# Optimization experiments

Hardware: AMD Instinct MI355X
Metric: run time of the kernel (lower is better)

The kernel has to match this reference:

```python
import jax, jax.numpy as jnp
import numpy as np

N = 100000; E = 1600000; G = 2000; S = 40; MAXP = 50
IN = 64; F = 128; H = 4; HD = F // H; FFN = 8 * F
EPS = 1e-5; BN_EPS = 1e-5

def _ln(x, g, b):
    m = jnp.mean(x, -1, keepdims=True)
    v = jnp.mean((x - m) ** 2, -1, keepdims=True)
    return (x - m) * jax.lax.rsqrt(v + EPS) * g + b

def setup_inputs():
    key = jax.random.key(0)
    ks = jax.random.split(key, 16)
    def lin(k, i, o):
        kw, kb = jax.random.split(k)
        lim = 1.0 / np.sqrt(i)
        return (jax.random.uniform(kw, (i, o), jnp.float32, -lim, lim),
                jax.random.uniform(kb, (o,), jnp.float32, -lim, lim))
    W_gcn, b_gcn = lin(ks[1], IN, F)
    Wq, bq = lin(ks[2], F, F); Wk, bk = lin(ks[3], F, F)
    Wv, bv = lin(ks[4], F, F); Wo, bo = lin(ks[5], F, F)
    W1, b1 = lin(ks[6], F, FFN); W2, b2 = lin(ks[7], FFN, F)
    Wg, bg = lin(ks[8], 2 * F, F)
    ones = lambda: jnp.ones((F,), jnp.float32)
    zeros = lambda: jnp.zeros((F,), jnp.float32)
    return {
        'x': jax.random.normal(ks[0], (N, IN), jnp.float32),
        'edge_index': jax.random.randint(ks[9], (2, E), 0, N),
        'batch': jnp.repeat(jnp.arange(G), N // G),
        'set_batch': jnp.repeat(jnp.arange(S), G // S),
        'W_gcn': W_gcn, 'b_gcn': b_gcn,
        'bn_g': ones(), 'bn_b': zeros(),
        'lnpre_g': ones(), 'lnpre_b': zeros(),
        'Wq': Wq, 'bq': bq, 'Wk': Wk, 'bk': bk, 'Wv': Wv, 'bv': bv, 'Wo': Wo, 'bo': bo,
        'ln1_g': ones(), 'ln1_b': zeros(),
        'W1': W1, 'b1': b1, 'W2': W2, 'b2': b2,
        'ln2_g': ones(), 'ln2_b': zeros(),
        'Wg': Wg, 'bg': bg,
    }

def _forward(x, W_gcn, b_gcn, bn_g, bn_b, lnpre_g, lnpre_b, Wq, bq, Wk, bk, Wv, bv, Wo, bo, ln1_g, ln1_b, W1, b1, W2, b2, ln2_g, ln2_b, Wg, bg, edge_index, batch, set_batch):
    row, col = edge_index[0], edge_index[1]
    # GCNConv, improved=True -> self-loop weight 2.0 (PyG gcn_norm)
    xw = x @ W_gcn                                              # [N,F]
    deg = jax.ops.segment_sum(jnp.ones(E, xw.dtype), col, N) + 2.0
    dinv = jax.lax.rsqrt(deg)
    norm = dinv[row] * dinv[col]                                # [E]
    agg = jax.ops.segment_sum(xw[row] * norm[:, None], col, N)  # scatter-add to targets
    h = agg + (2.0 * dinv * dinv)[:, None] * xw + b_gcn
    # BatchNorm1d eval (running_mean=0, running_var=1) + ReLU; dropout is identity in eval
    h = jax.nn.relu(h * jax.lax.rsqrt(jnp.asarray(1.0 + BN_EPS, h.dtype)) * bn_g + bn_b)
    # global mean pool per graph
    cnt_g = jax.ops.segment_sum(jnp.ones(N, h.dtype), batch, G)
    z = jax.ops.segment_sum(h, batch, G) / cnt_g[:, None]       # [G,F]
    # to_dense_batch over sets (set_batch is sorted)
    cnt_s = jax.ops.segment_sum(jnp.ones(G, jnp.int32), set_batch, S)
    starts = jnp.cumsum(cnt_s) - cnt_s
    pos = jnp.arange(G) - starts[set_batch]                     # position within set
    zd = jnp.zeros((S, MAXP, F), z.dtype).at[set_batch, pos].set(z)
    mask = jnp.arange(MAXP)[None, :] < cnt_s[:, None]           # [S,MAXP]
    # pre-LN MHA with key_padding_mask
    zn = _ln(zd, lnpre_g, lnpre_b)
    q = (zn @ Wq + bq).reshape(S, MAXP, H, HD)
    k = (zn @ Wk + bk).reshape(S, MAXP, H, HD)
    v = (zn @ Wv + bv).reshape(S, MAXP, H, HD)
    scores = jnp.einsum('sqhd,skhd->shqk', q, k) / np.sqrt(HD)
    scores = jnp.where(mask[:, None, None, :], scores, -1e9)
    attn = jax.nn.softmax(scores, -1)
    o = jnp.einsum('shqk,skhd->sqhd', attn, v).reshape(S, MAXP, F) @ Wo + bo
    zd = _ln(zd + o, ln1_g, ln1_b)
    # FFN block (post-LN residual)
    f = jax.nn.relu(zd @ W1 + b1) @ W2 + b2
    zd = _ln(zd + f, ln2_g, ln2_b)
    # z_dense[mask] ordering == gather via (set_batch, pos); broadcast to nodes
    set_info = zd[set_batch, pos][batch]                        # [N,F]
    # gated fusion
    gate = jax.nn.sigmoid(jnp.concatenate([h, set_info], -1) @ Wg + bg)
    return gate * set_info + (1.0 - gate) * h

def reference(x, edge_index, batch, set_batch, W_gcn, b_gcn, bn_g, bn_b, lnpre_g, lnpre_b, Wq, bq, Wk, bk, Wv, bv, Wo, bo, ln1_g, ln1_b, W1, b1, W2, b2, ln2_g, ln2_b, Wg, bg):
    return _forward(x, W_gcn, b_gcn, bn_g, bn_b, lnpre_g, lnpre_b, Wq, bq, Wk, bk, Wv, bv, Wo, bo, ln1_g, ln1_b, W1, b1, W2, b2, ln2_g, ln2_b, Wg, bg, edge_index, batch, set_batch)
```

## Files before the change

### kernel.cpp

```cpp
#include <hip/hip_runtime.h>
#include <hip/hip_bf16.h>
#include <cstddef>

#define NN 100000
#define NE 1600000
#define NG 2000
#define NS 40
#define INF 64
#define F 128
#define FFN_DIM 1024
#define NB 782
#define BCAP 3072
#define SC_BLOCKS 512
#define SC_CHUNK 3125
#define KSPLIT 8

using bf16 = __hip_bfloat16;
typedef __attribute__((ext_vector_type(8))) short short8;
typedef __attribute__((ext_vector_type(4))) float f32x4;
typedef __attribute__((ext_vector_type(2))) float f32x2;

__device__ __forceinline__ short f2bs(float f){
    union { bf16 b; short s; } u; u.b = __float2bfloat16(f); return u.s;
}
__device__ __forceinline__ unsigned int pk2(float a, float b){
    return (unsigned int)(unsigned short)f2bs(a) | ((unsigned int)(unsigned short)f2bs(b) << 16);
}

__global__ __launch_bounds__(1024) void k_binit(int* __restrict__ bcursor){
    int t = threadIdx.x;
    if (t < NB) bcursor[t] = t * BCAP;
}

__global__ __launch_bounds__(256) void k_xws(const float* __restrict__ x, const float* __restrict__ W,
                                             const float* __restrict__ dinv, unsigned char* __restrict__ xws8){
    __shared__ short Xs[128*72];
    __shared__ short Ws[128*72];
    int t = threadIdx.x;
    int rowBase = blockIdx.x * 128;
    #pragma unroll
    for (int i=0;i<32;i++){
        int id = i*256+t; int k = id>>7, n = id&127;
        Ws[n*72 + k] = f2bs(W[id]);
    }
    #pragma unroll
    for (int i=0;i<8;i++){
        int id = i*256+t;
        int r = id>>4; int k4 = (id&15)*4;
        int row = rowBase + r; if (row >= NN) row = NN-1;
        float4 v = *(const float4*)&x[(size_t)row*INF + k4];
        *(unsigned int*)&Xs[r*72 + k4]     = pk2(v.x, v.y);
        *(unsigned int*)&Xs[r*72 + k4 + 2] = pk2(v.z, v.w);
    }
    __syncthreads();
    int lane = t & 63, w = t >> 6;
    int lr = lane & 15, quad = lane >> 4;
    f32x4 acc[2][8];
    #pragma unroll
    for (int i=0;i<2;i++)
        #pragma unroll
        for (int j=0;j<8;j++) acc[i][j] = (f32x4){0.f,0.f,0.f,0.f};
    #pragma unroll
    for (int ks=0; ks<2; ++ks){
        int kb = ks*32 + quad*8;
        short8 b0 = *(const short8*)&Xs[((w  )*16 + lr)*72 + kb];
        short8 b1 = *(const short8*)&Xs[((w+4)*16 + lr)*72 + kb];
        #pragma unroll
        for (int mt=0; mt<8; ++mt){
            short8 a = *(const short8*)&Ws[(mt*16 + lr)*72 + kb];
            acc[0][mt] = __builtin_amdgcn_mfma_f32_16x16x32_bf16(a, b0, acc[0][mt], 0, 0, 0);
            acc[1][mt] = __builtin_amdgcn_mfma_f32_16x16x32_bf16(a, b1, acc[1][mt], 0, 0, 0);
        }
    }
    #pragma unroll
    for (int rt=0; rt<2; ++rt){
        int row = rowBase + (w + rt*4)*16 + lr;
        if (row < NN){
            float dv = dinv[row];
            #pragma unroll
            for (int mt=0; mt<8; ++mt){
                int p = __builtin_amdgcn_cvt_pk_fp8_f32(acc[rt][mt][0]*dv, acc[rt][mt][1]*dv, 0, false);
                p     = __builtin_amdgcn_cvt_pk_fp8_f32(acc[rt][mt][2]*dv, acc[rt][mt][3]*dv, p, true);
                *(int*)&xws8[(size_t)row*F + mt*16 + quad*4] = p;
            }
        }
    }
}

__global__ __launch_bounds__(1024) void k_scatter2(const int* __restrict__ ei, int* __restrict__ bcursor,
                                                   int* __restrict__ ebuf){
    __shared__ int lh[NB];
    __shared__ int lb[NB];
    int t = threadIdx.x;
    int base = blockIdx.x * SC_CHUNK;
    for (int b=t; b<NB; b+=1024) lh[b] = 0;
    __syncthreads();
    int rr[4], cc[4];
    #pragma unroll
    for (int q=0;q<4;q++){
        int i = t + q*1024;
        bool v = (i < SC_CHUNK);
        int idx = v ? (base + i) : base;
        rr[q] = ei[idx];
        cc[q] = ei[NE + idx];
        if (v) atomicAdd(&lh[cc[q]>>7], 1);
    }
    __syncthreads();
    for (int b=t; b<NB; b+=1024){
        int n = lh[b];
        lb[b] = n ? atomicAdd(&bcursor[b], n) : 0;
        lh[b] = 0;
    }
    __syncthreads();
    #pragma unroll
    for (int q=0;q<4;q++){
        int i = t + q*1024;
        if (i < SC_CHUNK){
            int b = cc[q] >> 7;
            int rk = atomicAdd(&lh[b], 1);
            ebuf[lb[b] + rk] = (rr[q] << 7) | (cc[q] & 127);
        }
    }
}

__global__ __launch_bounds__(256) void k_sort(const int* __restrict__ ebuf, const int* __restrict__ bcursor,
                                              int* __restrict__ cnt, float* __restrict__ dinv,
                                              int* __restrict__ nstart, int* __restrict__ ebuf2){
    __shared__ int lh[128];
    __shared__ int s[128];
    __shared__ int lcur[128];
    int t = threadIdx.x;
    int b = blockIdx.x;
    int e0 = b * BCAP;
    int nE = bcursor[b] - e0;
    if (t < 128) lh[t] = 0;
    __syncthreads();
    for (int i=t; i<nE; i+=256) atomicAdd(&lh[ebuf[e0+i] & 127], 1);
    __syncthreads();
    int c = (t < 128) ? lh[t] : 0;
    if (t < 128) s[t] = c;
    __syncthreads();
    #pragma unroll
    for (int off=1; off<128; off<<=1){
        int v = (t >= off && t < 128) ? s[t-off] : 0;
        __syncthreads();
        if (t < 128) s[t] += v;
        __syncthreads();
    }
    int node = b*128 + t;
    if (t < 128){
        int excl = s[t] - c;
        lcur[t] = excl;
        if (node < NN){
            nstart[node] = e0 + excl;
            cnt[node] = c;
            dinv[node] = rsqrtf((float)c + 2.0f);
        }
    }
    __syncthreads();
    for (int i=t; i<nE; i+=256){
        int v = ebuf[e0 + i];
        int nl = v & 127;
        int rk = atomicAdd(&lcur[nl], 1);
        ebuf2[e0 + rk] = (v >> 7) << 5;
    }
}

__global__ __launch_bounds__(256) void k_aggpool(const unsigned char* __restrict__ xws8,
                                                 const int* __restrict__ nstart, const int* __restrict__ cnt,
                                                 const float* __restrict__ dinv, const float* __restrict__ b_gcn,
                                                 const float* __restrict__ bn_g, const float* __restrict__ bn_b,
                                                 const int* __restrict__ ebuf2,
                                                 const float* __restrict__ lnpre_g, const float* __restrict__ lnpre_b,
                                                 float* __restrict__ h, unsigned short* __restrict__ hb,
                                                 float* __restrict__ z, float* __restrict__ zn,
                                                 unsigned short* __restrict__ znb){
    __shared__ float zacc[4][128];
    int t = threadIdx.x;
    int lane = t & 63, w = t >> 6;
    int half = lane >> 5, lh = lane & 31;
    int g = blockIdx.x;
    const unsigned int* xw32 = (const unsigned int*)xws8;
    unsigned int* hb32 = (unsigned int*)hb;
    unsigned int* znb32 = (unsigned int*)znb;

    float4 bg4  = *(const float4*)&b_gcn[4*lh];
    float4 bng4 = *(const float4*)&bn_g[4*lh];
    float4 bnb4 = *(const float4*)&bn_b[4*lh];
    const float bns = rsqrtf(1.f + 1e-5f);

    float za0=0.f, za1=0.f, za2=0.f, za3=0.f;

    for (int i = w; i < 50; i += 4){
        int node = g*50 + i;
        int s0n = nstart[node]; int dg = cnt[node]; float dv = dinv[node];
        unsigned int us = xw32[node*32 + lh];
        float a0=0.f, a1=0.f, a2=0.f, a3=0.f;
        int j=0;
        for (; j+8<=dg; j+=8){
            int r0 = ebuf2[s0n+j+0+half];
            int r1 = ebuf2[s0n+j+2+half];
            int r2 = ebuf2[s0n+j+4+half];
            int r3 = ebuf2[s0n+j+6+half];
            unsigned int u0 = xw32[r0 + lh];
            unsigned int u1 = xw32[r1 + lh];
            unsigned int u2 = xw32[r2 + lh];
            unsigned int u3 = xw32[r3 + lh];
            f32x2 l0 = __builtin_amdgcn_cvt_pk_f32_fp8(u0, false);
            f32x2 h0 = __builtin_amdgcn_cvt_pk_f32_fp8(u0, true);
            f32x2 l1 = __builtin_amdgcn_cvt_pk_f32_fp8(u1, false);
            f32x2 h1 = __builtin_amdgcn_cvt_pk_f32_fp8(u1, true);
            f32x2 l2 = __builtin_amdgcn_cvt_pk_f32_fp8(u2, false);
            f32x2 h2 = __builtin_amdgcn_cvt_pk_f32_fp8(u2, true);
            f32x2 l3 = __builtin_amdgcn_cvt_pk_f32_fp8(u3, false);
            f32x2 h3 = __builtin_amdgcn_cvt_pk_f32_fp8(u3, true);
            a0 += (l0.x + l1.x) + (l2.x + l3.x);
            a1 += (l0.y + l1.y) + (l2.y + l3.y);
            a2 += (h0.x + h1.x) + (h2.x + h3.x);
            a3 += (h0.y + h1.y) + (h2.y + h3.y);
        }
        for (; j+2<=dg; j+=2){
            int r0 = ebuf2[s0n+j+half];
            unsigned int u0 = xw32[r0 + lh];
            f32x2 l0 = __builtin_amdgcn_cvt_pk_f32_fp8(u0, false);
            f32x2 h0 = __builtin_amdgcn_cvt_pk_f32_fp8(u0, true);
            a0 += l0.x; a1 += l0.y; a2 += h0.x; a3 += h0.y;
        }
        if (j < dg && half == 0){
            int r0 = ebuf2[s0n+j];
            unsigned int u0 = xw32[r0 + lh];
            f32x2 l0 = __builtin_amdgcn_cvt_pk_f32_fp8(u0, false);
            f32x2 h0 = __builtin_amdgcn_cvt_pk_f32_fp8(u0, true);
            a0 += l0.x; a1 += l0.y; a2 += h0.x; a3 += h0.y;
        }
        a0 += __shfl_xor(a0, 32);
        a1 += __shfl_xor(a1, 32);
        a2 += __shfl_xor(a2, 32);
        a3 += __shfl_xor(a3, 32);
        f32x2 fl = __builtin_amdgcn_cvt_pk_f32_fp8(us, false);
        f32x2 fh = __builtin_amdgcn_cvt_pk_f32_fp8(us, true);
        float p0 = dv*(a0 + 2.f*fl.x) + bg4.x;
        float p1 = dv*(a1 + 2.f*fl.y) + bg4.y;
        float p2 = dv*(a2 + 2.f*fh.x) + bg4.z;
        float p3 = dv*(a3 + 2.f*fh.y) + bg4.w;
        p0 = fmaxf(p0*bns*bng4.x + bnb4.x, 0.f);
        p1 = fmaxf(p1*bns*bng4.y + bnb4.y, 0.f);
        p2 = fmaxf(p2*bns*bng4.z + bnb4.z, 0.f);
        p3 = fmaxf(p3*bns*bng4.w + bnb4.w, 0.f);
        if (half == 0){
            *(float4*)&h[(size_t)node*F + 4*lh] = make_float4(p0,p1,p2,p3);
            *(uint2*)&hb32[(size_t)node*64 + 2*lh] = make_uint2(pk2(p0,p1), pk2(p2,p3));
        }
        za0 += p0; za1 += p1; za2 += p2; za3 += p3;
    }
    if (half == 0)
        *(float4*)&zacc[w][4*lh] = make_float4(za0, za1, za2, za3);
    __syncthreads();
    if (w == 0){
        float4 v0 = *(const float4*)&zacc[0][4*lh];
        float4 v1 = *(const float4*)&zacc[1][4*lh];
        float4 v2 = *(const float4*)&zacc[2][4*lh];
        float4 v3 = *(const float4*)&zacc[3][4*lh];
        float s0 = ((v0.x+v1.x)+(v2.x+v3.x)) / 50.0f;
        float s1 = ((v0.y+v1.y)+(v2.y+v3.y)) / 50.0f;
        float s2 = ((v0.z+v1.z)+(v2.z+v3.z)) / 50.0f;
        float s3 = ((v0.w+v1.w)+(v2.w+v3.w)) / 50.0f;
        if (half == 0)
            *(float4*)&z[(size_t)g*F + 4*lh] = make_float4(s0,s1,s2,s3);
        float s = (s0+s1)+(s2+s3);
        #pragma unroll
        for (int off=1; off<32; off<<=1) s += __shfl_xor(s, off);
        float m = s * (1.f/128.f);
        float d0=s0-m, d1=s1-m, d2=s2-m, d3=s3-m;
        float vv = (d0*d0+d1*d1)+(d2*d2+d3*d3);
        #pragma unroll
        for (int off=1; off<32; off<<=1) vv += __shfl_xor(vv, off);
        float rs = rsqrtf(vv*(1.f/128.f) + 1e-5f);
        float4 lg = *(const float4*)&lnpre_g[4*lh];
        float4 lb = *(const float4*)&lnpre_b[4*lh];
        if (half == 0){
            float o0 = d0*rs*lg.x+lb.x, o1 = d1*rs*lg.y+lb.y;
            float o2 = d2*rs*lg.z+lb.z, o3 = d3*rs*lg.w+lb.w;
            *(float4*)&zn[(size_t)g*F + 4*lh] = make_float4(o0,o1,o2,o3);
            *(uint2*)&znb32[(size_t)g*64 + 2*lh] = make_uint2(pk2(o0,o1), pk2(o2,o3));
        }
    }
}

template<int RELU, int BF16OUT, int SPLITK>
__global__ __launch_bounds__(256) void k_mm_bf16(const unsigned short* __restrict__ A,
                                                 const float* __restrict__ B, const float* __restrict__ bias,
                                                 float* __restrict__ Cf, unsigned short* __restrict__ Cb,
                                                 int M, int K, int Nc){
    __shared__ short Bw[128*136];
    int t = threadIdx.x;
    int rowBase = blockIdx.x*128;
    int colBase = blockIdx.y*128;
    int kbeg = SPLITK ? blockIdx.z*128 : 0;
    #pragma unroll
    for (int i=0;i<64;i++){
        int id = i*256+t; int k = id>>7, n = id&127;
        Bw[n*136 + k] = f2bs(B[(size_t)(kbeg+k)*Nc + colBase + n]);
    }
    __syncthreads();
    int lane = t & 63, w = t >> 6;
    int lr = lane & 15, quad = lane >> 4;
    int mrow0 = rowBase + w*32;
    f32x4 acc[2][8];
    #pragma unroll
    for (int i=0;i<2;i++)
        #pragma unroll
        for (int j=0;j<8;j++) acc[i][j] = (f32x4){0.f,0.f,0.f,0.f};
    #pragma unroll
    for (int ks=0; ks<4; ++ks){
        int kb = ks*32 + quad*8;
        short8 a[2];
        #pragma unroll
        for (int mt=0; mt<2; ++mt){
            int row = mrow0 + mt*16 + lr;
            if (row >= M) row = M-1;
            a[mt] = *(const short8*)&A[(size_t)row*K + kbeg + kb];
        }
        #pragma unroll
        for (int nt=0; nt<8; ++nt){
            short8 b = *(const short8*)&Bw[(nt*16 + lr)*136 + kb];
            acc[0][nt] = __builtin_amdgcn_mfma_f32_16x16x32_bf16(a[0], b, acc[0][nt], 0, 0, 0);
            acc[1][nt] = __builtin_amdgcn_mfma_f32_16x16x32_bf16(a[1], b, acc[1][nt], 0, 0, 0);
        }
    }
    #pragma unroll
    for (int mt=0; mt<2; ++mt){
        #pragma unroll
        for (int r=0; r<4; ++r){
            int row = mrow0 + mt*16 + quad*4 + r;
            if (row >= M) continue;
            #pragma unroll
            for (int nt=0; nt<8; ++nt){
                int col = colBase + nt*16 + lr;
                float v = acc[mt][nt][r];
                if (!SPLITK){
                    v += bias[col];
                    if (RELU) v = fmaxf(v, 0.f);
                    if (BF16OUT) Cb[(size_t)row*Nc + col] = (unsigned short)f2bs(v);
                    else         Cf[(size_t)row*Nc + col] = v;
                } else {
                    Cf[(size_t)blockIdx.z*M*Nc + (size_t)row*Nc + col] = v;
                }
            }
        }
    }
}

__global__ __launch_bounds__(256) void k_qkv_mfma(const unsigned short* __restrict__ A,
                                                  const float* __restrict__ Wq, const float* __restrict__ Wk,
                                                  const float* __restrict__ Wv, const float* __restrict__ bq,
                                                  const float* __restrict__ bk, const float* __restrict__ bv,
                                                  float* __restrict__ Cq, float* __restrict__ Ck,
                                                  float* __restrict__ Cv){
    __shared__ short Bw[128*136];
    int t = threadIdx.x;
    int zsel = blockIdx.z;
    const float* B = (zsel==0) ? Wq : (zsel==1) ? Wk : Wv;
    const float* bias = (zsel==0) ? bq : (zsel==1) ? bk : bv;
    float* C = (zsel==0) ? Cq : (zsel==1) ? Ck : Cv;
    int rowBase = blockIdx.x*128;
    #pragma unroll
    for (int i=0;i<64;i++){
        int id = i*256+t; int k = id>>7, n = id&127;
        Bw[n*136 + k] = f2bs(B[(size_t)k*F + n]);
    }
    __syncthreads();
    int lane = t & 63, w = t >> 6;
    int lr = lane & 15, quad = lane >> 4;
    int mrow0 = rowBase + w*32;
    f32x4 acc[2][8];
    #pragma unroll
    for (int i=0;i<2;i++)
        #pragma unroll
        for (int j=0;j<8;j++) acc[i][j] = (f32x4){0.f,0.f,0.f,0.f};
    #pragma unroll
    for (int ks=0; ks<4; ++ks){
        int kb = ks*32 + quad*8;
        short8 a[2];
        #pragma unroll
        for (int mt=0; mt<2; ++mt){
            int row = mrow0 + mt*16 + lr;
            if (row >= NG) row = NG-1;
            a[mt] = *(const short8*)&A[(size_t)row*F + kb];
        }
        #pragma unroll
        for (int nt=0; nt<8; ++nt){
            short8 b = *(const short8*)&Bw[(nt*16 + lr)*136 + kb];
            acc[0][nt] = __builtin_amdgcn_mfma_f32_16x16x32_bf16(a[0], b, acc[0][nt], 0, 0, 0);
            acc[1][nt] = __builtin_amdgcn_mfma_f32_16x16x32_bf16(a[1], b, acc[1][nt], 0, 0, 0);
        }
    }
    #pragma unroll
    for (int mt=0; mt<2; ++mt){
        #pragma unroll
        for (int r=0; r<4; ++r){
            int row = mrow0 + mt*16 + quad*4 + r;
            if (row >= NG) continue;
            #pragma unroll
            for (int nt=0; nt<8; ++nt){
                int col = nt*16 + lr;
                C[(size_t)row*F + col] = acc[mt][nt][r] + bias[col];
            }
        }
    }
}

__global__ __launch_bounds__(256) void k_wo_ln(const float* __restrict__ ao, const float* __restrict__ Wo,
                                               const float* __restrict__ bo, const float* __restrict__ z,
                                               const float* __restrict__ g, const float* __restrict__ b,
                                               float* __restrict__ zd1, unsigned short* __restrict__ zd1b){
    __shared__ float As[32*36];
    __shared__ float Bs[32*128];
    int t = threadIdx.x;
    int rowBase = blockIdx.x*32;
    int c0 = (t&31)*4, r0 = (t>>5)*4;
    unsigned int* zd1b32 = (unsigned int*)zd1b;
    float acc[4][4];
    #pragma unroll
    for (int i=0;i<4;i++){ acc[i][0]=0.f; acc[i][1]=0.f; acc[i][2]=0.f; acc[i][3]=0.f; }
    for (int kb=0; kb<F; kb+=32){
        #pragma unroll
        for (int i=0;i<4;i++){
            int id = i*256+t; int kk = id&31; int r = id>>5;
            int row = rowBase + r;
            As[kk*36+r] = (row<NG) ? ao[(size_t)row*F + kb + kk] : 0.f;
        }
        #pragma unroll
        for (int i=0;i<16;i++){
            int id = i*256+t; int c = id&127; int kk = id>>7;
            Bs[kk*128+c] = Wo[(size_t)(kb+kk)*F + c];
        }
        __syncthreads();
        for (int kk=0;kk<32;kk++){
            float4 a = *(const float4*)&As[kk*36+r0];
            float4 bv = *(const float4*)&Bs[kk*128+c0];
            float av[4]={a.x,a.y,a.z,a.w}; float bb[4]={bv.x,bv.y,bv.z,bv.w};
            #pragma unroll
            for(int i=0;i<4;i++)
                #pragma unroll
                for(int j=0;j<4;j++) acc[i][j] += av[i]*bb[j];
        }
        __syncthreads();
    }
    float4 bo4 = *(const float4*)&bo[c0];
    float4 g4  = *(const float4*)&g[c0];
    float4 b4  = *(const float4*)&b[c0];
    #pragma unroll
    for (int i=0;i<4;i++){
        int row = rowBase + r0 + i;
        float v0=0.f,v1=0.f,v2=0.f,v3=0.f;
        if (row < NG){
            float4 zr = *(const float4*)&z[(size_t)row*F + c0];
            v0 = acc[i][0] + bo4.x + zr.x;
            v1 = acc[i][1] + bo4.y + zr.y;
            v2 = acc[i][2] + bo4.z + zr.z;
            v3 = acc[i][3] + bo4.w + zr.w;
        }
        float s = (v0+v1)+(v2+v3);
        #pragma unroll
        for (int off=1; off<32; off<<=1) s += __shfl_xor(s, off);
        float m = s * (1.f/128.f);
        float d0=v0-m, d1=v1-m, d2=v2-m, d3=v3-m;
        float vv = (d0*d0+d1*d1)+(d2*d2+d3*d3);
        #pragma unroll
        for (int off=1; off<32; off<<=1) vv += __shfl_xor(vv, off);
        float rs = rsqrtf(vv*(1.f/128.f) + 1e-5f);
        if (row < NG){
            float o0 = d0*rs*g4.x+b4.x, o1 = d1*rs*g4.y+b4.y;
            float o2 = d2*rs*g4.z+b4.z, o3 = d3*rs*g4.w+b4.w;
            *(float4*)&zd1[(size_t)row*F + c0] = make_float4(o0,o1,o2,o3);
            *(uint2*)&zd1b32[(size_t)row*(F/2) + c0/2] = make_uint2(pk2(o0,o1), pk2(o2,o3));
        }
    }
}

__global__ __launch_bounds__(256) void k_ln_red_gsi(const float* __restrict__ A, const float* __restrict__ part,
                                                    const float* __restrict__ bias, const float* __restrict__ g,
                                                    const float* __restrict__ b, const float* __restrict__ Wb,
                                                    const float* __restrict__ bg, float* __restrict__ zd2,
                                                    float* __restrict__ gsi){
    __shared__ float Zs[4][128];
    __shared__ float Bs[32*128];
    int t = threadIdx.x; int lane = t&63;
    int rquad = t>>6;
    int row = blockIdx.x*4 + rquad;
    int i0 = row*F + 2*lane;
    float x0 = A[i0] + bias[2*lane], x1 = A[i0+1] + bias[2*lane+1];
    #pragma unroll
    for (int zz=0; zz<KSPLIT; ++zz){
        x0 += part[(size_t)zz*NG*F + i0];
        x1 += part[(size_t)zz*NG*F + i0 + 1];
    }
    float s = x0+x1;
    for (int off=1; off<64; off<<=1) s += __shfl_xor(s, off);
    float m = s * (1.f/128.f);
    float d0 = x0-m, d1 = x1-m;
    float vv = d0*d0 + d1*d1;
    for (int off=1; off<64; off<<=1) vv += __shfl_xor(vv, off);
    float rs = rsqrtf(vv*(1.f/128.f) + 1e-5f);
    float o0 = d0*rs*g[2*lane]   + b[2*lane];
    float o1 = d1*rs*g[2*lane+1] + b[2*lane+1];
    zd2[i0]   = o0;
    zd2[i0+1] = o1;
    Zs[rquad][2*lane]   = o0;
    Zs[rquad][2*lane+1] = o1;
    __syncthreads();
    int col = t & 127, rp = t >> 7;
    float a0=0.f, a1=0.f;
    for (int kb=0; kb<F; kb+=32){
        #pragma unroll
        for (int i=0;i<16;i++){
            int id = i*256+t; int c = id&127; int kk = id>>7;
            Bs[kk*128+c] = Wb[(size_t)(kb+kk)*F + c];
        }
        __syncthreads();
        for (int kk=0;kk<32;kk++){
            float w = Bs[kk*128+col];
            a0 += Zs[rp][kb+kk]   * w;
            a1 += Zs[rp+2][kb+kk] * w;
        }
        __syncthreads();
    }
    float bgc = bg[col];
    gsi[(size_t)(blockIdx.x*4 + rp)*F + col]     = a0 + bgc;
    gsi[(size_t)(blockIdx.x*4 + rp + 2)*F + col] = a1 + bgc;
}

__global__ __launch_bounds__(256) void k_attn(const float* __restrict__ q, const float* __restrict__ k,
                                              const float* __restrict__ v, float* __restrict__ o){
    __shared__ float Qs[1600], Ks[1600], Vs[1600], Sc[2500];
    int t = threadIdx.x;
    int s = blockIdx.x >> 2; int hh = blockIdx.x & 3;
    for (int idx=t; idx<1600; idx+=256){
        int i = idx>>5, d = idx&31;
        size_t gi = (size_t)(s*50+i)*F + hh*32 + d;
        Qs[idx]=q[gi]; Ks[idx]=k[gi]; Vs[idx]=v[gi];
    }
    __syncthreads();
    for (int idx=t; idx<2500; idx+=256){
        int qi = idx/50, ki = idx%50;
        float acc=0.f;
        #pragma unroll 8
        for (int d=0;d<32;d++) acc += Qs[qi*32+d]*Ks[ki*32+d];
        Sc[idx] = acc * 0.17677669529663687f;
    }
    __syncthreads();
    if (t < 50){
        float m=-1e30f;
        for (int j=0;j<50;j++) m = fmaxf(m, Sc[t*50+j]);
        float sum=0.f;
        for (int j=0;j<50;j++){ float e=__expf(Sc[t*50+j]-m); Sc[t*50+j]=e; sum+=e; }
        float inv = 1.f/sum;
        for (int j=0;j<50;j++) Sc[t*50+j] *= inv;
    }
    __syncthreads();
    for (int idx=t; idx<1600; idx+=256){
        int qi = idx>>5, d = idx&31;
        float acc=0.f;
        #pragma unroll 10
        for (int ki=0;ki<50;ki++) acc += Sc[qi*50+ki]*Vs[ki*32+d];
        o[(size_t)(s*50+qi)*F + hh*32 + d] = acc;
    }
}

__global__ __launch_bounds__(256) void k_gate_mfma(const float* __restrict__ h,
                                                   const unsigned short* __restrict__ hb,
                                                   const float* __restrict__ Wg,
                                                   const float* __restrict__ gsi, const float* __restrict__ zd2,
                                                   float* __restrict__ out){
    __shared__ short Bw[128*136];
    int t = threadIdx.x;
    for (int i=t; i<16384; i+=256){
        int k = i >> 7, n = i & 127;
        Bw[n*136 + k] = f2bs(Wg[(size_t)k*F + n]);
    }
    __syncthreads();
    int lane = t & 63, w = t >> 6;
    int lr = lane & 15, quad = lane >> 4;
    int mrow0 = blockIdx.x*128 + w*32;
    f32x4 acc[2][8];
    #pragma unroll
    for (int i=0;i<2;i++)
        #pragma unroll
        for (int j=0;j<8;j++) acc[i][j] = (f32x4){0.f,0.f,0.f,0.f};
    #pragma unroll
    for (int ks=0; ks<4; ++ks){
        int kb = ks*32 + quad*8;
        short8 a[2];
        #pragma unroll
        for (int mt=0; mt<2; ++mt){
            int row = mrow0 + mt*16 + lr;
            if (row >= NN) row = NN-1;
            a[mt] = *(const short8*)&hb[(size_t)row*F + kb];
        }
        #pragma unroll
        for (int nt=0; nt<8; ++nt){
            short8 b = *(const short8*)&Bw[(nt*16 + lr)*136 + kb];
            acc[0][nt] = __builtin_amdgcn_mfma_f32_16x16x32_bf16(a[0], b, acc[0][nt], 0, 0, 0);
            acc[1][nt] = __builtin_amdgcn_mfma_f32_16x16x32_bf16(a[1], b, acc[1][nt], 0, 0, 0);
        }
    }
    #pragma unroll
    for (int mt=0; mt<2; ++mt){
        #pragma unroll
        for (int r=0; r<4; ++r){
            int row = mrow0 + mt*16 + quad*4 + r;
            if (row >= NN) continue;
            int g = row / 50;
            const float* gs = &gsi[(size_t)g*F];
            const float* zs = &zd2[(size_t)g*F];
            const float* hr = &h[(size_t)row*F];
            float* orow = &out[(size_t)row*F];
            #pragma unroll
            for (int nt=0; nt<8; ++nt){
                int col = nt*16 + lr;
                float L = acc[mt][nt][r] + gs[col];
                float gate = 1.f/(1.f + __expf(-L));
                orow[col] = gate*zs[col] + (1.f-gate)*hr[col];
            }
        }
    }
}

extern "C" void kernel_launch(void* const* d_in, const int* in_sizes, int n_in,
                              void* d_out, int out_size, void* d_ws, size_t ws_size,
                              hipStream_t stream) {
    const float* x      = (const float*)d_in[0];
    const int*   ei     = (const int*)d_in[1];
    const float* W_gcn  = (const float*)d_in[4];
    const float* b_gcn  = (const float*)d_in[5];
    const float* bn_g   = (const float*)d_in[6];
    const float* bn_b   = (const float*)d_in[7];
    const float* lnpre_g= (const float*)d_in[8];
    const float* lnpre_b= (const float*)d_in[9];
    const float* Wq     = (const float*)d_in[10];
    const float* bq     = (const float*)d_in[11];
    const float* Wk     = (const float*)d_in[12];
    const float* bk     = (const float*)d_in[13];
    const float* Wv     = (const float*)d_in[14];
    const float* bv     = (const float*)d_in[15];
    const float* Wo     = (const float*)d_in[16];
    const float* bo     = (const float*)d_in[17];
    const float* ln1_g  = (const float*)d_in[18];
    const float* ln1_b  = (const float*)d_in[19];
    const float* W1     = (const float*)d_in[20];
    const float* b1     = (const float*)d_in[21];
    const float* W2     = (const float*)d_in[22];
    const float* b2     = (const float*)d_in[23];
    const float* ln2_g  = (const float*)d_in[24];
    const float* ln2_b  = (const float*)d_in[25];
    const float* Wg     = (const float*)d_in[26];
    const float* bg     = (const float*)d_in[27];
    float* out = (float*)d_out;
    char* ws = (char*)d_ws;

    size_t o = 0;
    unsigned char* xws8 = (unsigned char*)(ws + o); o += (size_t)NN*F;
    float* h     = (float*)(ws + o); o += (size_t)NN*F*4;
    unsigned short* hb = (unsigned short*)(ws + o); o += (size_t)NN*F*2;
    int*   cnt   = (int*)(ws + o);   o += (size_t)NN*4;
    int*   nstart= (int*)(ws + o);   o += (size_t)NN*4;
    int*   ebuf  = (int*)(ws + o);   o += (size_t)NB*BCAP*4;
    int*   ebuf2 = (int*)(ws + o);   o += (size_t)NB*BCAP*4;
    float* dinv  = (float*)(ws + o); o += (size_t)NN*4;
    int*   bcursor=(int*)(ws + o);   o += 1024*4;
    float* z     = (float*)(ws + o); o += (size_t)NG*F*4;
    float* zn    = (float*)(ws + o); o += (size_t)NG*F*4;
    unsigned short* znb = (unsigned short*)(ws + o); o += (size_t)NG*F*2;
    float* qb    = (float*)(ws + o); o += (size_t)NG*F*4;
    float* kb2   = (float*)(ws + o); o += (size_t)NG*F*4;
    float* vb    = (float*)(ws + o); o += (size_t)NG*F*4;
    float* ao    = (float*)(ws + o); o += (size_t)NG*F*4;
    float* zd1   = (float*)(ws + o); o += (size_t)NG*F*4;
    unsigned short* zd1b = (unsigned short*)(ws + o); o += (size_t)NG*F*2;
    unsigned short* ffn1b = (unsigned short*)(ws + o); o += (size_t)NG*FFN_DIM*2;
    float* part  = (float*)(ws + o); o += (size_t)KSPLIT*NG*F*4;
    float* zd2   = (float*)(ws + o); o += (size_t)NG*F*4;
    float* gsi   = (float*)(ws + o); o += (size_t)NG*F*4;

    k_binit<<<1, 1024, 0, stream>>>(bcursor);
    k_scatter2<<<SC_BLOCKS, 1024, 0, stream>>>(ei, bcursor, ebuf);
    k_sort<<<NB, 256, 0, stream>>>(ebuf, bcursor, cnt, dinv, nstart, ebuf2);
    k_xws<<<(NN+127)/128, 256, 0, stream>>>(x, W_gcn, dinv, xws8);
    k_aggpool<<<NG, 256, 0, stream>>>(xws8, nstart, cnt, dinv, b_gcn, bn_g, bn_b, ebuf2,
                                      lnpre_g, lnpre_b, h, hb, z, zn, znb);

    dim3 gqkv((NG+127)/128, 1, 3);
    k_qkv_mfma<<<gqkv, 256, 0, stream>>>(znb, Wq, Wk, Wv, bq, bk, bv, qb, kb2, vb);
    k_attn<<<NS*4, 256, 0, stream>>>(qb, kb2, vb, ao);
    k_wo_ln<<<(NG+31)/32, 256, 0, stream>>>(ao, Wo, bo, z, ln1_g, ln1_b, zd1, zd1b);
    dim3 gffn1((NG+127)/128, FFN_DIM/128, 1);
    k_mm_bf16<1,1,0><<<gffn1, 256, 0, stream>>>(zd1b, W1, b1, nullptr, ffn1b, NG, F, FFN_DIM);
    dim3 gffn2((NG+127)/128, 1, KSPLIT);
    k_mm_bf16<0,0,1><<<gffn2, 256, 0, stream>>>(ffn1b, W2, nullptr, part, nullptr, NG, FFN_DIM, F);
    k_ln_red_gsi<<<NG/4, 256, 0, stream>>>(zd1, part, b2, ln2_g, ln2_b,
                                           Wg + (size_t)F*F, bg, zd2, gsi);

    k_gate_mfma<<<782, 256, 0, stream>>>(h, hb, Wg, gsi, zd2, out);
}
```

Baseline: 354.0 us.

## Pre-convert gate weights to bf16 once and read B directly from global

Adds a small kernel that converts and transposes the gate-weight half Wg into a bf16 buffer once per call. The gate kernel then loads B fragments straight from global memory (cache-resident) instead of every block staging and converting a 128x128 tile into shared memory. The gate kernel's tile also shrinks from 128 to 64 rows per block, doubling the block count and dropping LDS use to raise occupancy. The cost is an extra launch and less A/B reuse per wave, since B is re-read from cache for each 16-row tile.

```diff
diff --git a/kernel.cpp b/kernel.cpp
--- a/kernel.cpp
+++ b/kernel.cpp
@@ -30,6 +30,14 @@
 __global__ __launch_bounds__(1024) void k_binit(int* __restrict__ bcursor){
     int t = threadIdx.x;
     if (t < NB) bcursor[t] = t * BCAP;
+}
+
+__global__ __launch_bounds__(256) void k_wcvt(const float* __restrict__ Wg, unsigned short* __restrict__ Wgb){
+    int t = blockIdx.x*256 + threadIdx.x;
+    for (int i=t; i<16384; i+=16*256){
+        int k = i >> 7, n = i & 127;
+        Wgb[n*128 + k] = (unsigned short)f2bs(Wg[(size_t)k*F + n]);
+    }
 }
 
 __global__ __launch_bounds__(256) void k_xws(const float* __restrict__ x, const float* __restrict__ W,
@@ -570,59 +578,43 @@
 
 __global__ __launch_bounds__(256) void k_gate_mfma(const float* __restrict__ h,
                                                    const unsigned short* __restrict__ hb,
-                                                   const float* __restrict__ Wg,
+                                                   const unsigned short* __restrict__ Wgb,
                                                    const float* __restrict__ gsi, const float* __restrict__ zd2,
                                                    float* __restrict__ out){
-    __shared__ short Bw[128*136];
-    int t = threadIdx.x;
-    for (int i=t; i<16384; i+=256){
-        int k = i >> 7, n = i & 127;
-        Bw[n*136 + k] = f2bs(Wg[(size_t)k*F + n]);
-    }
-    __syncthreads();
+    int t = threadIdx.x;
     int lane = t & 63, w = t >> 6;
     int lr = lane & 15, quad = lane >> 4;
-    int mrow0 = blockIdx.x*128 + w*32;
-    f32x4 acc[2][8];
-    #pragma unroll
-    for (int i=0;i<2;i++)
-        #pragma unroll
-        for (int j=0;j<8;j++) acc[i][j] = (f32x4){0.f,0.f,0.f,0.f};
+    int mrow0 = blockIdx.x*64 + w*16;
+    f32x4 acc[8];
+    #pragma unroll
+    for (int j=0;j<8;j++) acc[j] = (f32x4){0.f,0.f,0.f,0.f};
     #pragma unroll
     for (int ks=0; ks<4; ++ks){
         int kb = ks*32 + quad*8;
-        short8 a[2];
-        #pragma unroll
-        for (int mt=0; mt<2; ++mt){
-            int row = mrow0 + mt*16 + lr;
-            if (row >= NN) row = NN-1;
-            a[mt] = *(const short8*)&hb[(size_t)row*F + kb];
-        }
+        int row = mrow0 + lr;
+        if (row >= NN) row = NN-1;
+        short8 a = *(const short8*)&hb[(size_t)row*F + kb];
         #pragma unroll
         for (int nt=0; nt<8; ++nt){
-            short8 b = *(const short8*)&Bw[(nt*16 + lr)*136 + kb];
-            acc[0][nt] = __builtin_amdgcn_mfma_f32_16x16x32_bf16(a[0], b, acc[0][nt], 0, 0, 0);
-            acc[1][nt] = __builtin_amdgcn_mfma_f32_16x16x32_bf16(a[1], b, acc[1][nt], 0, 0, 0);
-        }
-    }
-    #pragma unroll
-    for (int mt=0; mt<2; ++mt){
-        #pragma unroll
-        for (int r=0; r<4; ++r){
-            int row = mrow0 + mt*16 + quad*4 + r;
-            if (row >= NN) continue;
-            int g = row / 50;
-            const float* gs = &gsi[(size_t)g*F];
-            const float* zs = &zd2[(size_t)g*F];
-            const float* hr = &h[(size_t)row*F];
-            float* orow = &out[(size_t)row*F];
-            #pragma unroll
-            for (int nt=0; nt<8; ++nt){
-                int col = nt*16 + lr;
-                float L = acc[mt][nt][r] + gs[col];
-                float gate = 1.f/(1.f + __expf(-L));
-                orow[col] = gate*zs[col] + (1.f-gate)*hr[col];
-            }
+            short8 b = *(const short8*)&Wgb[(size_t)(nt*16 + lr)*128 + kb];
+            acc[nt] = __builtin_amdgcn_mfma_f32_16x16x32_bf16(a, b, acc[nt], 0, 0, 0);
+        }
+    }
+    #pragma unroll
+    for (int r=0; r<4; ++r){
+        int row = mrow0 + quad*4 + r;
+        if (row >= NN) continue;
+        int g = row / 50;
+        const float* gs = &gsi[(size_t)g*F];
+        const float* zs = &zd2[(size_t)g*F];
+        const float* hr = &h[(size_t)row*F];
+        float* orow = &out[(size_t)row*F];
+        #pragma unroll
+        for (int nt=0; nt<8; ++nt){
+            int col = nt*16 + lr;
+            float L = acc[nt][r] + gs[col];
+            float gate = 1.f/(1.f + __expf(-L));
+            orow[col] = gate*zs[col] + (1.f-gate)*hr[col];
         }
     }
 }
@@ -669,6 +661,7 @@
     int*   ebuf2 = (int*)(ws + o);   o += (size_t)NB*BCAP*4;
     float* dinv  = (float*)(ws + o); o += (size_t)NN*4;
     int*   bcursor=(int*)(ws + o);   o += 1024*4;
+    unsigned short* Wgb = (unsigned short*)(ws + o); o += 16384*2;
     float* z     = (float*)(ws + o); o += (size_t)NG*F*4;
     float* zn    = (float*)(ws + o); o += (size_t)NG*F*4;
     unsigned short* znb = (unsigned short*)(ws + o); o += (size_t)NG*F*2;
@@ -684,6 +677,7 @@
     float* gsi   = (float*)(ws + o); o += (size_t)NG*F*4;
 
     k_binit<<<1, 1024, 0, stream>>>(bcursor);
+    k_wcvt<<<16, 256, 0, stream>>>(Wg, Wgb);
     k_scatter2<<<SC_BLOCKS, 1024, 0, stream>>>(ei, bcursor, ebuf);
     k_sort<<<NB, 256, 0, stream>>>(ebuf, bcursor, cnt, dinv, nstart, ebuf2);
     k_xws<<<(NN+127)/128, 256, 0, stream>>>(x, W_gcn, dinv, xws8);
@@ -701,5 +695,5 @@
     k_ln_red_gsi<<<NG/4, 256, 0, stream>>>(zd1, part, b2, ln2_g, ln2_b,
                                            Wg + (size_t)F*F, bg, zd2, gsi);
 
-    k_gate_mfma<<<782, 256, 0, stream>>>(h, hb, Wg, gsi, zd2, out);
-}
+    k_gate_mfma<<<(NN+63)/64, 256, 0, stream>>>(h, hb, Wgb, gsi, zd2, out);
+}
```

Result: no change. 351.9 us (-0.6%).
